# Kernel optimization log

Hardware: AMD Instinct MI355X
Metric: run time of the kernel (lower is better)

The kernel has to match this reference:

```python
import jax, jax.numpy as jnp
import numpy as np

K = 2            # number of attention heads (k in __init__)
NEG = -9.0e15    # mask fill value from the torch code
N, C, CO = 6144, 128, 128


def _ln(x, g, b, eps=1e-5):
    m = x.mean(-1, keepdims=True)
    v = ((x - m) ** 2).mean(-1, keepdims=True)
    return (x - m) / jnp.sqrt(v + eps) * g + b


def setup_inputs() -> dict:
    key = jax.random.key(0)
    ks = jax.random.split(key, 6)
    x = jax.random.normal(ks[0], (N, C), jnp.float32)
    adj = (jax.random.uniform(ks[1], (N, N)) < 0.01).astype(jnp.float32)
    ff0_w = jax.random.normal(ks[2], (K, C, C), jnp.float32) / np.float32(np.sqrt(C))
    ff1_w = jax.random.normal(ks[3], (K, CO, C), jnp.float32) / np.float32(np.sqrt(C))
    attn_w = jax.random.normal(ks[4], (K, 2 * C), jnp.float32) / np.float32(np.sqrt(2 * C))
    return dict(
        x=x, adj=adj, ff0_w=ff0_w, ff1_w=ff1_w, attn_w=attn_w,
        g1=jnp.ones((C,), jnp.float32), b1=jnp.zeros((C,), jnp.float32),
        g2=jnp.ones((C,), jnp.float32), b2=jnp.zeros((C,), jnp.float32),
    )


def reference(x, adj, ff0_w, ff1_w, attn_w, g1, b1, g2, b2):
    n, c = x.shape
    co = ff1_w.shape[1]
    x_norm = _ln(x, g1, b1)
    # torch does adj = adj + eye(n) each iteration; since adj >= 0 the mask
    # (adj > 0) is identical for every iteration: original edges plus self-loops.
    mask = (adj > 0) | jnp.eye(n, dtype=bool)
    h_next = jnp.zeros((n, co), x.dtype)
    for i in range(K):  # small fixed head count, structurally distinct weights
        h = x_norm @ ff0_w[i].T  # [n, c]
        # attn_fc(cat(h_i, h_j)) == a1.h_i + a2.h_j  (exact decomposition of
        # the concat+linear; avoids materializing the [n, n, 2c] tensor)
        s_src = h @ attn_w[i, :c]  # [n], contribution of row node i
        s_dst = h @ attn_w[i, c:]  # [n], contribution of col node j
        e = jax.nn.leaky_relu(s_src[:, None] + s_dst[None, :])  # [n, n]
        e = jnp.where(mask, e, jnp.float32(NEG))
        atten = jax.nn.softmax(e, axis=1)  # dropout p=0.0 -> identity
        att = atten @ h + x  # residual adds pre-norm x
        att = _ln(att, g2, b2)
        h_next = h_next + jax.nn.elu(att @ ff1_w[i].T) / K
    return h_next
```

## Files before the change

### kernel.cpp

```cpp
#include <hip/hip_runtime.h>
#include <math.h>

#define Nn 6144
#define Cc 128
#define NHD 2
#define MAXDEG 1024

__device__ __forceinline__ float wave_red_sum(float v) {
#pragma unroll
  for (int o = 32; o; o >>= 1) v += __shfl_xor(v, o);
  return v;
}

template <bool IS_MAX>
__device__ __forceinline__ void block_red2(float& a, float& b, float* red) {
#pragma unroll
  for (int o = 32; o; o >>= 1) {
    float ta = __shfl_xor(a, o), tb = __shfl_xor(b, o);
    if (IS_MAX) { a = fmaxf(a, ta); b = fmaxf(b, tb); }
    else        { a += ta;          b += tb;          }
  }
  int wid = threadIdx.x >> 6;
  __syncthreads();
  if ((threadIdx.x & 63) == 0) { red[wid] = a; red[4 + wid] = b; }
  __syncthreads();
  if (IS_MAX) {
    a = fmaxf(fmaxf(red[0], red[1]), fmaxf(red[2], red[3]));
    b = fmaxf(fmaxf(red[4], red[5]), fmaxf(red[6], red[7]));
  } else {
    a = red[0] + red[1] + red[2] + red[3];
    b = red[4] + red[5] + red[6] + red[7];
  }
}

__global__ __launch_bounds__(256) void k_ln(const float* __restrict__ x,
                                            const float* __restrict__ g,
                                            const float* __restrict__ b,
                                            float* __restrict__ xn) {
  int wid = threadIdx.x >> 6, lane = threadIdx.x & 63;
  int row = blockIdx.x * 4 + wid;
  float2 v = ((const float2*)(x + (size_t)row * Cc))[lane];
  float s = v.x + v.y;
#pragma unroll
  for (int o = 32; o; o >>= 1) s += __shfl_xor(s, o);
  float mean = s * (1.0f / Cc);
  float dx = v.x - mean, dy = v.y - mean;
  float q = dx * dx + dy * dy;
#pragma unroll
  for (int o = 32; o; o >>= 1) q += __shfl_xor(q, o);
  float rstd = rsqrtf(q * (1.0f / Cc) + 1e-5f);
  int c = lane * 2;
  float* o = xn + (size_t)row * Cc;
  o[c]     = dx * rstd * g[c] + b[c];
  o[c + 1] = dy * rstd * g[c + 1] + b[c + 1];
}

__global__ __launch_bounds__(256) void k_gemm_ff0(const float* __restrict__ A,
                                                  const float* __restrict__ Bw,
                                                  float* __restrict__ out) {
  __shared__ float As[64][68];
  __shared__ float Bs[64][132];
  const int t = threadIdx.x;
  const int head = blockIdx.y;
  const int row0 = blockIdx.x * 64;
  const float* Bh = Bw + (size_t)head * Cc * Cc;
  const int tr = t & 15, tc = t >> 4;
  const int r0 = tr * 4, c0 = tc * 8;
  float acc[4][8];
#pragma unroll
  for (int i = 0; i < 4; i++)
#pragma unroll
    for (int j = 0; j < 8; j++) acc[i][j] = 0.f;

  for (int kt = 0; kt < Cc; kt += 64) {
    __syncthreads();
    for (int i = t; i < 1024; i += 256) {
      int rr = i >> 4, k4 = i & 15;
      float4 v = *(const float4*)(A + (size_t)(row0 + rr) * Cc + kt + k4 * 4);
      As[k4 * 4 + 0][rr] = v.x; As[k4 * 4 + 1][rr] = v.y;
      As[k4 * 4 + 2][rr] = v.z; As[k4 * 4 + 3][rr] = v.w;
    }
    for (int i = t; i < 2048; i += 256) {
      int cc2 = i >> 4, k4 = i & 15;
      float4 v = *(const float4*)(Bh + (size_t)cc2 * Cc + kt + k4 * 4);
      Bs[k4 * 4 + 0][cc2] = v.x; Bs[k4 * 4 + 1][cc2] = v.y;
      Bs[k4 * 4 + 2][cc2] = v.z; Bs[k4 * 4 + 3][cc2] = v.w;
    }
    __syncthreads();
#pragma unroll
    for (int k = 0; k < 64; k++) {
      float4 a  = *(const float4*)&As[k][r0];
      float4 b0 = *(const float4*)&Bs[k][c0];
      float4 b1 = *(const float4*)&Bs[k][c0 + 4];
      float av[4] = {a.x, a.y, a.z, a.w};
      float bv[8] = {b0.x, b0.y, b0.z, b0.w, b1.x, b1.y, b1.z, b1.w};
#pragma unroll
      for (int i = 0; i < 4; i++)
#pragma unroll
        for (int j = 0; j < 8; j++) acc[i][j] = fmaf(av[i], bv[j], acc[i][j]);
    }
  }
#pragma unroll
  for (int i = 0; i < 4; i++) {
    float* op = out + ((size_t)head * Nn + row0 + r0 + i) * Cc + c0;
    *(float4*)(op)     = make_float4(acc[i][0], acc[i][1], acc[i][2], acc[i][3]);
    *(float4*)(op + 4) = make_float4(acc[i][4], acc[i][5], acc[i][6], acc[i][7]);
  }
}

__global__ __launch_bounds__(256) void k_gemm_ff1(const float* __restrict__ A,
                                                  const float* __restrict__ Bw,
                                                  float* __restrict__ out) {
  __shared__ float As[64][68];
  __shared__ float Bs[64][132];
  const int t = threadIdx.x;
  const int row0 = blockIdx.x * 64;
  const int tr = t & 15, tc = t >> 4;
  const int r0 = tr * 4, c0 = tc * 8;
  float sum[4][8];
#pragma unroll
  for (int i = 0; i < 4; i++)
#pragma unroll
    for (int j = 0; j < 8; j++) sum[i][j] = 0.f;

  for (int head = 0; head < NHD; head++) {
    const float* Ah = A + (size_t)head * Nn * Cc;
    const float* Bh = Bw + (size_t)head * Cc * Cc;
    float acc[4][8];
#pragma unroll
    for (int i = 0; i < 4; i++)
#pragma unroll
      for (int j = 0; j < 8; j++) acc[i][j] = 0.f;

    for (int kt = 0; kt < Cc; kt += 64) {
      __syncthreads();
      for (int i = t; i < 1024; i += 256) {
        int rr = i >> 4, k4 = i & 15;
        float4 v = *(const float4*)(Ah + (size_t)(row0 + rr) * Cc + kt + k4 * 4);
        As[k4 * 4 + 0][rr] = v.x; As[k4 * 4 + 1][rr] = v.y;
        As[k4 * 4 + 2][rr] = v.z; As[k4 * 4 + 3][rr] = v.w;
      }
      for (int i = t; i < 2048; i += 256) {
        int cc2 = i >> 4, k4 = i & 15;
        float4 v = *(const float4*)(Bh + (size_t)cc2 * Cc + kt + k4 * 4);
        Bs[k4 * 4 + 0][cc2] = v.x; Bs[k4 * 4 + 1][cc2] = v.y;
        Bs[k4 * 4 + 2][cc2] = v.z; Bs[k4 * 4 + 3][cc2] = v.w;
      }
      __syncthreads();
#pragma unroll
      for (int k = 0; k < 64; k++) {
        float4 a  = *(const float4*)&As[k][r0];
        float4 b0 = *(const float4*)&Bs[k][c0];
        float4 b1 = *(const float4*)&Bs[k][c0 + 4];
        float av[4] = {a.x, a.y, a.z, a.w};
        float bv[8] = {b0.x, b0.y, b0.z, b0.w, b1.x, b1.y, b1.z, b1.w};
#pragma unroll
        for (int i = 0; i < 4; i++)
#pragma unroll
          for (int j = 0; j < 8; j++) acc[i][j] = fmaf(av[i], bv[j], acc[i][j]);
      }
    }
#pragma unroll
    for (int i = 0; i < 4; i++)
#pragma unroll
      for (int j = 0; j < 8; j++) {
        float v = acc[i][j];
        v = (v > 0.f) ? v : (expf(v) - 1.f);
        sum[i][j] = fmaf(v, 0.5f, sum[i][j]);
      }
  }
#pragma unroll
  for (int i = 0; i < 4; i++) {
    float* op = out + (size_t)(row0 + r0 + i) * Cc + c0;
    *(float4*)(op)     = make_float4(sum[i][0], sum[i][1], sum[i][2], sum[i][3]);
    *(float4*)(op + 4) = make_float4(sum[i][4], sum[i][5], sum[i][6], sum[i][7]);
  }
}

__global__ __launch_bounds__(256) void k_attn_s(const float* __restrict__ h,
                                                const float* __restrict__ aw,
                                                float* __restrict__ ssrc,
                                                float* __restrict__ sdst) {
  int wid = threadIdx.x >> 6, lane = threadIdx.x & 63;
  int row = blockIdx.x * 4 + wid;
#pragma unroll
  for (int hd = 0; hd < NHD; hd++) {
    float2 v  = ((const float2*)(h + ((size_t)hd * Nn + row) * Cc))[lane];
    float2 w1 = ((const float2*)(aw + hd * 2 * Cc))[lane];
    float2 w2 = ((const float2*)(aw + hd * 2 * Cc + Cc))[lane];
    float a = v.x * w1.x + v.y * w1.y;
    float b = v.x * w2.x + v.y * w2.y;
#pragma unroll
    for (int o = 32; o; o >>= 1) { a += __shfl_xor(a, o); b += __shfl_xor(b, o); }
    if (lane == 0) { ssrc[hd * Nn + row] = a; sdst[hd * Nn + row] = b; }
  }
}

__global__ __launch_bounds__(256) void k_attn(
    const float* __restrict__ adj, const float* __restrict__ x,
    const float* __restrict__ h, const float* __restrict__ ssrc,
    const float* __restrict__ sdst, const float* __restrict__ g2,
    const float* __restrict__ b2, float* __restrict__ att_out) {
  __shared__ __align__(16) int nbr[MAXDEG];
  __shared__ __align__(16) float wts[NHD][MAXDEG];
  __shared__ float red[8];
  __shared__ int cnt;
  const int t = threadIdx.x;
  const int r = blockIdx.x;
  if (t == 0) cnt = 0;
  __syncthreads();
  const float4* arow = (const float4*)(adj + (size_t)r * Nn);
  for (int i = t; i < Nn / 4; i += 256) {
    float4 v = arow[i];
    int j = i * 4;
    if (v.x > 0.f || j + 0 == r) { int p = atomicAdd(&cnt, 1); if (p < MAXDEG) nbr[p] = j + 0; }
    if (v.y > 0.f || j + 1 == r) { int p = atomicAdd(&cnt, 1); if (p < MAXDEG) nbr[p] = j + 1; }
    if (v.z > 0.f || j + 2 == r) { int p = atomicAdd(&cnt, 1); if (p < MAXDEG) nbr[p] = j + 2; }
    if (v.w > 0.f || j + 3 == r) { int p = atomicAdd(&cnt, 1); if (p < MAXDEG) nbr[p] = j + 3; }
  }
  __syncthreads();
  const int deg = min(cnt, MAXDEG);
  const float s0 = ssrc[r], s1 = ssrc[Nn + r];
  float m0 = -3.0e38f, m1 = -3.0e38f;
  for (int k = t; k < deg; k += 256) {
    int j = nbr[k];
    float e0 = s0 + sdst[j];
    float e1 = s1 + sdst[Nn + j];
    e0 = (e0 > 0.f) ? e0 : 0.01f * e0;
    e1 = (e1 > 0.f) ? e1 : 0.01f * e1;
    wts[0][k] = e0; wts[1][k] = e1;
    m0 = fmaxf(m0, e0); m1 = fmaxf(m1, e1);
  }
  block_red2<true>(m0, m1, red);
  float l0 = 0.f, l1 = 0.f;
  for (int k = t; k < deg; k += 256) {
    float w0 = __expf(wts[0][k] - m0); wts[0][k] = w0; l0 += w0;
    float w1 = __expf(wts[1][k] - m1); wts[1][k] = w1; l1 += w1;
  }
  block_red2<false>(l0, l1, red);
  {
    const int hd = t >> 7, g = (t >> 5) & 3, c4 = t & 31;
    const float* hp = h + (size_t)hd * Nn * Cc + c4 * 4;
    float4 a4 = make_float4(0.f, 0.f, 0.f, 0.f);
#pragma unroll 2
    for (int k = g; k < deg; k += 4) {
      float w = wts[hd][k];
      const float4 hv = *(const float4*)(hp + (size_t)nbr[k] * Cc);
      a4.x = fmaf(w, hv.x, a4.x);
      a4.y = fmaf(w, hv.y, a4.y);
      a4.z = fmaf(w, hv.z, a4.z);
      a4.w = fmaf(w, hv.w, a4.w);
    }
    __syncthreads();
    float4* part = (float4*)&wts[0][0];
    part[t] = a4;
    __syncthreads();
    float* attbuf = (float*)nbr;
    if (t < 64) {
      const int hd2 = t >> 5, cb = t & 31;
      float4 p0 = part[hd2 * 128 + 0  + cb];
      float4 p1 = part[hd2 * 128 + 32 + cb];
      float4 p2 = part[hd2 * 128 + 64 + cb];
      float4 p3 = part[hd2 * 128 + 96 + cb];
      float sx_ = p0.x + p1.x + p2.x + p3.x;
      float sy_ = p0.y + p1.y + p2.y + p3.y;
      float sz_ = p0.z + p1.z + p2.z + p3.z;
      float sw_ = p0.w + p1.w + p2.w + p3.w;
      const float inv2 = 1.0f / (hd2 ? l1 : l0);
      const float4 xv = *(const float4*)(x + (size_t)r * Cc + cb * 4);
      float4 att4;
      att4.x = fmaf(sx_, inv2, xv.x);
      att4.y = fmaf(sy_, inv2, xv.y);
      att4.z = fmaf(sz_, inv2, xv.z);
      att4.w = fmaf(sw_, inv2, xv.w);
      ((float4*)attbuf)[hd2 * 32 + cb] = att4;
    }
    __syncthreads();
    const int c = t & 127;
    float att = attbuf[(t >> 7) * 128 + c];
    float s = wave_red_sum(att);
    int wid = t >> 6;
    __syncthreads();
    if ((t & 63) == 0) red[wid] = s;
    __syncthreads();
    float mean = (red[(t >> 7) * 2] + red[(t >> 7) * 2 + 1]) * (1.0f / Cc);
    float d = att - mean;
    float q = wave_red_sum(d * d);
    __syncthreads();
    if ((t & 63) == 0) red[wid] = q;
    __syncthreads();
    float var = (red[(t >> 7) * 2] + red[(t >> 7) * 2 + 1]) * (1.0f / Cc);
    float rstd = rsqrtf(var + 1e-5f);
    att_out[((size_t)(t >> 7) * Nn + r) * Cc + c] = d * rstd * g2[c] + b2[c];
  }
}

extern "C" void kernel_launch(void* const* d_in, const int* in_sizes, int n_in,
                              void* d_out, int out_size, void* d_ws, size_t ws_size,
                              hipStream_t stream) {
  const float* x   = (const float*)d_in[0];
  const float* adj = (const float*)d_in[1];
  const float* ff0 = (const float*)d_in[2];
  const float* ff1 = (const float*)d_in[3];
  const float* aw  = (const float*)d_in[4];
  const float* g1  = (const float*)d_in[5];
  const float* b1  = (const float*)d_in[6];
  const float* g2  = (const float*)d_in[7];
  const float* b2  = (const float*)d_in[8];
  float* out = (float*)d_out;

  float* ws    = (float*)d_ws;
  float* xnorm = ws;
  float* h     = xnorm + (size_t)Nn * Cc;
  float* ssrc  = h + (size_t)2 * Nn * Cc;
  float* sdst  = ssrc + 2 * Nn;
  float* attn  = sdst + 2 * Nn;

  hipLaunchKernelGGL(k_ln, dim3(Nn / 4), dim3(256), 0, stream, x, g1, b1, xnorm);
  hipLaunchKernelGGL(k_gemm_ff0, dim3(Nn / 64, 2), dim3(256), 0, stream, xnorm, ff0, h);
  hipLaunchKernelGGL(k_attn_s, dim3(Nn / 4), dim3(256), 0, stream, h, aw, ssrc, sdst);
  hipLaunchKernelGGL(k_attn, dim3(Nn), dim3(256), 0, stream, adj, x, h, ssrc, sdst, g2, b2, attn);
  hipLaunchKernelGGL(k_gemm_ff1, dim3(Nn / 64), dim3(256), 0, stream, attn, ff1, out);
}
```

Baseline: 311.1 us.

## Fuse LayerNorm, ff0 GEMM and attention score projection into one kernel

Folds the input LayerNorm into the ff0 GEMM prologue, keeping normalized rows in shared memory, and computes the src/dst attention scores in the GEMM epilogue through a shared-memory partial reduction. This removes two kernel launches and the xnorm and h re-reads. Both GEMMs move to 32-row tiles with 4x4 per-thread outputs, which doubles the block count but lowers per-thread register reuse. The total time is likely dominated by the dense-adjacency attention kernel, which is unchanged.

```diff
diff --git a/kernel.cpp b/kernel.cpp
--- a/kernel.cpp
+++ b/kernel.cpp
@@ -33,53 +33,56 @@
   }
 }
 
-__global__ __launch_bounds__(256) void k_ln(const float* __restrict__ x,
-                                            const float* __restrict__ g,
-                                            const float* __restrict__ b,
-                                            float* __restrict__ xn) {
-  int wid = threadIdx.x >> 6, lane = threadIdx.x & 63;
-  int row = blockIdx.x * 4 + wid;
-  float2 v = ((const float2*)(x + (size_t)row * Cc))[lane];
-  float s = v.x + v.y;
-#pragma unroll
-  for (int o = 32; o; o >>= 1) s += __shfl_xor(s, o);
-  float mean = s * (1.0f / Cc);
-  float dx = v.x - mean, dy = v.y - mean;
-  float q = dx * dx + dy * dy;
-#pragma unroll
-  for (int o = 32; o; o >>= 1) q += __shfl_xor(q, o);
-  float rstd = rsqrtf(q * (1.0f / Cc) + 1e-5f);
-  int c = lane * 2;
-  float* o = xn + (size_t)row * Cc;
-  o[c]     = dx * rstd * g[c] + b[c];
-  o[c + 1] = dy * rstd * g[c + 1] + b[c + 1];
-}
-
-__global__ __launch_bounds__(256) void k_gemm_ff0(const float* __restrict__ A,
-                                                  const float* __restrict__ Bw,
-                                                  float* __restrict__ out) {
-  __shared__ float As[64][68];
+__global__ __launch_bounds__(256) void k_ff0_fused(
+    const float* __restrict__ x, const float* __restrict__ g1,
+    const float* __restrict__ b1, const float* __restrict__ Bw,
+    const float* __restrict__ aw, float* __restrict__ h,
+    float* __restrict__ ssrc, float* __restrict__ sdst) {
+  __shared__ float Axn[128][36];
   __shared__ float Bs[64][132];
   const int t = threadIdx.x;
   const int head = blockIdx.y;
-  const int row0 = blockIdx.x * 64;
+  const int row0 = blockIdx.x * 32;
   const float* Bh = Bw + (size_t)head * Cc * Cc;
-  const int tr = t & 15, tc = t >> 4;
-  const int r0 = tr * 4, c0 = tc * 8;
-  float acc[4][8];
+
+  {
+    const int row = t >> 3, seg = t & 7;
+    const int cb = seg * 16;
+    const float* xr = x + (size_t)(row0 + row) * Cc + cb;
+    float v[16], gg[16], bb[16];
+#pragma unroll
+    for (int i = 0; i < 16; i += 4) {
+      float4 t4 = *(const float4*)(xr + i);
+      v[i] = t4.x; v[i + 1] = t4.y; v[i + 2] = t4.z; v[i + 3] = t4.w;
+      float4 g4 = *(const float4*)(g1 + cb + i);
+      gg[i] = g4.x; gg[i + 1] = g4.y; gg[i + 2] = g4.z; gg[i + 3] = g4.w;
+      float4 b4 = *(const float4*)(b1 + cb + i);
+      bb[i] = b4.x; bb[i + 1] = b4.y; bb[i + 2] = b4.z; bb[i + 3] = b4.w;
+    }
+    float s = 0.f;
+#pragma unroll
+    for (int i = 0; i < 16; i++) s += v[i];
+    s += __shfl_xor(s, 1); s += __shfl_xor(s, 2); s += __shfl_xor(s, 4);
+    float mean = s * (1.0f / 128.0f);
+    float q = 0.f;
+#pragma unroll
+    for (int i = 0; i < 16; i++) { float d_ = v[i] - mean; q += d_ * d_; }
+    q += __shfl_xor(q, 1); q += __shfl_xor(q, 2); q += __shfl_xor(q, 4);
+    float rstd = rsqrtf(q * (1.0f / 128.0f) + 1e-5f);
+#pragma unroll
+    for (int i = 0; i < 16; i++)
+      Axn[cb + i][row] = (v[i] - mean) * rstd * gg[i] + bb[i];
+  }
+  __syncthreads();
+
+  const int tr = t & 7, tc = t >> 3;
+  float acc[4][4];
 #pragma unroll
   for (int i = 0; i < 4; i++)
 #pragma unroll
-    for (int j = 0; j < 8; j++) acc[i][j] = 0.f;
+    for (int j = 0; j < 4; j++) acc[i][j] = 0.f;
 
   for (int kt = 0; kt < Cc; kt += 64) {
-    __syncthreads();
-    for (int i = t; i < 1024; i += 256) {
-      int rr = i >> 4, k4 = i & 15;
-      float4 v = *(const float4*)(A + (size_t)(row0 + rr) * Cc + kt + k4 * 4);
-      As[k4 * 4 + 0][rr] = v.x; As[k4 * 4 + 1][rr] = v.y;
-      As[k4 * 4 + 2][rr] = v.z; As[k4 * 4 + 3][rr] = v.w;
-    }
     for (int i = t; i < 2048; i += 256) {
       int cc2 = i >> 4, k4 = i & 15;
       float4 v = *(const float4*)(Bh + (size_t)cc2 * Cc + kt + k4 * 4);
@@ -89,52 +92,72 @@
     __syncthreads();
 #pragma unroll
     for (int k = 0; k < 64; k++) {
-      float4 a  = *(const float4*)&As[k][r0];
-      float4 b0 = *(const float4*)&Bs[k][c0];
-      float4 b1 = *(const float4*)&Bs[k][c0 + 4];
-      float av[4] = {a.x, a.y, a.z, a.w};
-      float bv[8] = {b0.x, b0.y, b0.z, b0.w, b1.x, b1.y, b1.z, b1.w};
+      float4 a4 = *(const float4*)&Axn[kt + k][tr * 4];
+      float4 b4 = *(const float4*)&Bs[k][tc * 4];
+      float av[4] = {a4.x, a4.y, a4.z, a4.w};
+      float bv[4] = {b4.x, b4.y, b4.z, b4.w};
 #pragma unroll
       for (int i = 0; i < 4; i++)
 #pragma unroll
-        for (int j = 0; j < 8; j++) acc[i][j] = fmaf(av[i], bv[j], acc[i][j]);
-    }
-  }
+        for (int j = 0; j < 4; j++) acc[i][j] = fmaf(av[i], bv[j], acc[i][j]);
+    }
+    __syncthreads();
+  }
+
+  float psrc[4], pdst[4];
+  {
+    float4 w1 = *(const float4*)(aw + head * 2 * Cc + tc * 4);
+    float4 w2 = *(const float4*)(aw + head * 2 * Cc + Cc + tc * 4);
+#pragma unroll
+    for (int i = 0; i < 4; i++) {
+      float* op = h + ((size_t)head * Nn + row0 + tr * 4 + i) * Cc + tc * 4;
+      *(float4*)op = make_float4(acc[i][0], acc[i][1], acc[i][2], acc[i][3]);
+      psrc[i] = acc[i][0] * w1.x + acc[i][1] * w1.y + acc[i][2] * w1.z + acc[i][3] * w1.w;
+      pdst[i] = acc[i][0] * w2.x + acc[i][1] * w2.y + acc[i][2] * w2.z + acc[i][3] * w2.w;
+    }
+  }
+  float* epart = &Bs[0][0];
 #pragma unroll
   for (int i = 0; i < 4; i++) {
-    float* op = out + ((size_t)head * Nn + row0 + r0 + i) * Cc + c0;
-    *(float4*)(op)     = make_float4(acc[i][0], acc[i][1], acc[i][2], acc[i][3]);
-    *(float4*)(op + 4) = make_float4(acc[i][4], acc[i][5], acc[i][6], acc[i][7]);
-  }
-}
-
-__global__ __launch_bounds__(256) void k_gemm_ff1(const float* __restrict__ A,
+    epart[((tc * 32) + (tr * 4 + i)) * 2 + 0] = psrc[i];
+    epart[((tc * 32) + (tr * 4 + i)) * 2 + 1] = pdst[i];
+  }
+  __syncthreads();
+  if (t < 64) {
+    int row = t >> 1, s = t & 1;
+    float v = 0.f;
+#pragma unroll
+    for (int g = 0; g < 32; g++) v += epart[(g * 32 + row) * 2 + s];
+    (s ? sdst : ssrc)[head * Nn + row0 + row] = v;
+  }
+}
+
+__global__ __launch_bounds__(256) void k_ff1_comb(const float* __restrict__ A,
                                                   const float* __restrict__ Bw,
                                                   float* __restrict__ out) {
-  __shared__ float As[64][68];
+  __shared__ float As[64][36];
   __shared__ float Bs[64][132];
   const int t = threadIdx.x;
-  const int row0 = blockIdx.x * 64;
-  const int tr = t & 15, tc = t >> 4;
-  const int r0 = tr * 4, c0 = tc * 8;
-  float sum[4][8];
+  const int row0 = blockIdx.x * 32;
+  const int tr = t & 7, tc = t >> 3;
+  float sum[4][4];
 #pragma unroll
   for (int i = 0; i < 4; i++)
 #pragma unroll
-    for (int j = 0; j < 8; j++) sum[i][j] = 0.f;
+    for (int j = 0; j < 4; j++) sum[i][j] = 0.f;
 
   for (int head = 0; head < NHD; head++) {
     const float* Ah = A + (size_t)head * Nn * Cc;
     const float* Bh = Bw + (size_t)head * Cc * Cc;
-    float acc[4][8];
+    float acc[4][4];
 #pragma unroll
     for (int i = 0; i < 4; i++)
 #pragma unroll
-      for (int j = 0; j < 8; j++) acc[i][j] = 0.f;
+      for (int j = 0; j < 4; j++) acc[i][j] = 0.f;
 
     for (int kt = 0; kt < Cc; kt += 64) {
       __syncthreads();
-      for (int i = t; i < 1024; i += 256) {
+      for (int i = t; i < 512; i += 256) {
         int rr = i >> 4, k4 = i & 15;
         float4 v = *(const float4*)(Ah + (size_t)(row0 + rr) * Cc + kt + k4 * 4);
         As[k4 * 4 + 0][rr] = v.x; As[k4 * 4 + 1][rr] = v.y;
@@ -149,21 +172,20 @@
       __syncthreads();
 #pragma unroll
       for (int k = 0; k < 64; k++) {
-        float4 a  = *(const float4*)&As[k][r0];
-        float4 b0 = *(const float4*)&Bs[k][c0];
-        float4 b1 = *(const float4*)&Bs[k][c0 + 4];
-        float av[4] = {a.x, a.y, a.z, a.w};
-        float bv[8] = {b0.x, b0.y, b0.z, b0.w, b1.x, b1.y, b1.z, b1.w};
+        float4 a4 = *(const float4*)&As[k][tr * 4];
+        float4 b4 = *(const float4*)&Bs[k][tc * 4];
+        float av[4] = {a4.x, a4.y, a4.z, a4.w};
+        float bv[4] = {b4.x, b4.y, b4.z, b4.w};
 #pragma unroll
         for (int i = 0; i < 4; i++)
 #pragma unroll
-          for (int j = 0; j < 8; j++) acc[i][j] = fmaf(av[i], bv[j], acc[i][j]);
+          for (int j = 0; j < 4; j++) acc[i][j] = fmaf(av[i], bv[j], acc[i][j]);
       }
     }
 #pragma unroll
     for (int i = 0; i < 4; i++)
 #pragma unroll
-      for (int j = 0; j < 8; j++) {
+      for (int j = 0; j < 4; j++) {
         float v = acc[i][j];
         v = (v > 0.f) ? v : (expf(v) - 1.f);
         sum[i][j] = fmaf(v, 0.5f, sum[i][j]);
@@ -171,28 +193,8 @@
   }
 #pragma unroll
   for (int i = 0; i < 4; i++) {
-    float* op = out + (size_t)(row0 + r0 + i) * Cc + c0;
-    *(float4*)(op)     = make_float4(sum[i][0], sum[i][1], sum[i][2], sum[i][3]);
-    *(float4*)(op + 4) = make_float4(sum[i][4], sum[i][5], sum[i][6], sum[i][7]);
-  }
-}
-
-__global__ __launch_bounds__(256) void k_attn_s(const float* __restrict__ h,
-                                                const float* __restrict__ aw,
-                                                float* __restrict__ ssrc,
-                                                float* __restrict__ sdst) {
-  int wid = threadIdx.x >> 6, lane = threadIdx.x & 63;
-  int row = blockIdx.x * 4 + wid;
-#pragma unroll
-  for (int hd = 0; hd < NHD; hd++) {
-    float2 v  = ((const float2*)(h + ((size_t)hd * Nn + row) * Cc))[lane];
-    float2 w1 = ((const float2*)(aw + hd * 2 * Cc))[lane];
-    float2 w2 = ((const float2*)(aw + hd * 2 * Cc + Cc))[lane];
-    float a = v.x * w1.x + v.y * w1.y;
-    float b = v.x * w2.x + v.y * w2.y;
-#pragma unroll
-    for (int o = 32; o; o >>= 1) { a += __shfl_xor(a, o); b += __shfl_xor(b, o); }
-    if (lane == 0) { ssrc[hd * Nn + row] = a; sdst[hd * Nn + row] = b; }
+    float* op = out + (size_t)(row0 + tr * 4 + i) * Cc + tc * 4;
+    *(float4*)op = make_float4(sum[i][0], sum[i][1], sum[i][2], sum[i][3]);
   }
 }
 
@@ -309,16 +311,14 @@
   const float* b2  = (const float*)d_in[8];
   float* out = (float*)d_out;
 
-  float* ws    = (float*)d_ws;
-  float* xnorm = ws;
-  float* h     = xnorm + (size_t)Nn * Cc;
-  float* ssrc  = h + (size_t)2 * Nn * Cc;
-  float* sdst  = ssrc + 2 * Nn;
-  float* attn  = sdst + 2 * Nn;
-
-  hipLaunchKernelGGL(k_ln, dim3(Nn / 4), dim3(256), 0, stream, x, g1, b1, xnorm);
-  hipLaunchKernelGGL(k_gemm_ff0, dim3(Nn / 64, 2), dim3(256), 0, stream, xnorm, ff0, h);
-  hipLaunchKernelGGL(k_attn_s, dim3(Nn / 4), dim3(256), 0, stream, h, aw, ssrc, sdst);
+  float* ws   = (float*)d_ws;
+  float* h    = ws;
+  float* ssrc = h + (size_t)2 * Nn * Cc;
+  float* sdst = ssrc + 2 * Nn;
+  float* attn = sdst + 2 * Nn;
+
+  hipLaunchKernelGGL(k_ff0_fused, dim3(Nn / 32, NHD), dim3(256), 0, stream,
+                     x, g1, b1, ff0, aw, h, ssrc, sdst);
   hipLaunchKernelGGL(k_attn, dim3(Nn), dim3(256), 0, stream, adj, x, h, ssrc, sdst, g2, b2, attn);
-  hipLaunchKernelGGL(k_gemm_ff1, dim3(Nn / 64), dim3(256), 0, stream, attn, ff1, out);
-}
+  hipLaunchKernelGGL(k_ff1_comb, dim3(Nn / 32), dim3(256), 0, stream, attn, ff1, out);
+}
```

New measurement: 295.1 us. -5.1%, faster.
